# Kernel tuning notes

Measured on AMD Instinct MI355X. Metric: run time of the kernel, lower is better.

## Reference

```python
import jax, jax.numpy as jnp
import numpy as np

HIDDEN = 1024
N_EXPERTS = 8
CAP_FACTOR = 1.1
LN_EPS = 1e-5


def setup_inputs() -> dict:
    key = jax.random.key(0)
    ks = jax.random.split(key, 8)
    d, E, dff = HIDDEN, N_EXPERTS, 4 * HIDDEN
    x = jax.random.normal(ks[0], (4, 2048, d), dtype=jnp.float32)
    gate_w = jax.random.normal(ks[1], (d, E), dtype=jnp.float32) / np.sqrt(d)
    ln_g = jnp.ones((E, d), dtype=jnp.float32)
    ln_b = jnp.zeros((E, d), dtype=jnp.float32)
    w1 = jax.random.normal(ks[2], (E, d, dff), dtype=jnp.float32) / np.sqrt(d)
    b1 = jnp.zeros((E, dff), dtype=jnp.float32)
    w2 = jax.random.normal(ks[3], (E, dff, d), dtype=jnp.float32) / np.sqrt(dff)
    b2 = jnp.zeros((E, d), dtype=jnp.float32)
    return {"x": x, "gate_w": gate_w, "ln_g": ln_g, "ln_b": ln_b,
            "w1": w1, "b1": b1, "w2": w2, "b2": b2}


def reference(x, gate_w, ln_g, ln_b, w1, b1, w2, b2):
    B, S, d = x.shape
    E = gate_w.shape[1]
    N = B * S
    cap = int(N / E * CAP_FACTOR)  # expert capacity

    xt = x.reshape(N, d)
    # Router: top-1 expert per token (max-subtract before softmax is a no-op)
    logits = xt @ gate_w                               # [N, E]
    probs = jax.nn.softmax(logits, axis=-1)
    eidx = jnp.argmax(probs, axis=-1)                  # [N] int

    onehot = jax.nn.one_hot(eidx, E, dtype=jnp.int32)  # [N, E]
    counts = onehot.sum(axis=0).astype(jnp.float32)    # pre-drop counts [E]

    # Deterministic capacity: keep first `cap` tokens per expert, drop rest.
    # (torch code drops randomly via multinomial; structure is identical.)
    pos = jnp.cumsum(onehot, axis=0) - 1               # [N, E]
    pos_tok = jnp.take_along_axis(pos, eidx[:, None], axis=1)[:, 0]  # [N]
    keep = (pos_tok < cap).astype(x.dtype)             # [N]
    pos_c = jnp.minimum(pos_tok, cap - 1)              # clamp; dropped tokens write zeros

    # Dispatch into per-expert buffers [E, cap, d]
    buf = jnp.zeros((E, cap, d), dtype=x.dtype).at[eidx, pos_c].add(xt * keep[:, None])

    # Per-expert FFN: LayerNorm -> Linear -> GELU -> Linear
    mu = buf.mean(axis=-1, keepdims=True)
    var = jnp.mean((buf - mu) ** 2, axis=-1, keepdims=True)
    nb = (buf - mu) * jax.lax.rsqrt(var + LN_EPS)
    nb = nb * ln_g[:, None, :] + ln_b[:, None, :]
    h = jax.nn.gelu(jnp.einsum('ecd,edf->ecf', nb, w1) + b1[:, None, :], approximate=False)
    y = jnp.einsum('ecf,efd->ecd', h, w2) + b2[:, None, :]  # [E, cap, d]

    # Combine: dropped tokens get zeros (matches torch output init)
    out_tok = y[eidx, pos_c] * keep[:, None]           # [N, d]
    output = out_tok.reshape(B, S, d)

    # Load-balancing loss: 1 - cosine(counts, uniform) * 0.01
    tokens_per_expert = N / E
    uniform = jnp.full((E,), tokens_per_expert, dtype=jnp.float32)
    cos = jnp.dot(counts, uniform) / (jnp.linalg.norm(counts) * jnp.linalg.norm(uniform) + 1e-8)
    loss = 1.0 - cos * 0.01
    return output, loss
```

## Files before the change

### kernel.cpp

```cpp
#include <hip/hip_runtime.h>
#include <cstdint>
#include <cstddef>

#define NTOK 8192
#define D    1024
#define DFF  4096
#define NEXP 8
#define CAP  1126
#define MPAD 1152

typedef float f32x4 __attribute__((ext_vector_type(4)));
typedef __bf16 bf16x8 __attribute__((ext_vector_type(8)));

__device__ inline unsigned short f2bf(float f) {
    unsigned u = __float_as_uint(f);
    u += 0x7fffu + ((u >> 16) & 1u);
    return (unsigned short)(u >> 16);
}

__device__ inline void gload16(const void* g, void* l) {
    __builtin_amdgcn_global_load_lds(
        (const __attribute__((address_space(1))) unsigned int*)g,
        (__attribute__((address_space(3))) unsigned int*)l,
        16, 0, 0);
}

__global__ __launch_bounds__(256) void router_kernel(
    const float* __restrict__ x, const float* __restrict__ gw, int* __restrict__ eidx)
{
    int tok  = blockIdx.x * 4 + (threadIdx.x >> 6);
    int lane = threadIdx.x & 63;
    const float* xr = x + (size_t)tok * D;
    float a[8] = {0.f,0.f,0.f,0.f,0.f,0.f,0.f,0.f};
    #pragma unroll
    for (int it = 0; it < D / 64; ++it) {
        int d = lane + it * 64;
        float xv = xr[d];
        const float4 g0 = *(const float4*)(gw + (size_t)d * 8);
        const float4 g1 = *(const float4*)(gw + (size_t)d * 8 + 4);
        a[0] += xv * g0.x; a[1] += xv * g0.y; a[2] += xv * g0.z; a[3] += xv * g0.w;
        a[4] += xv * g1.x; a[5] += xv * g1.y; a[6] += xv * g1.z; a[7] += xv * g1.w;
    }
    #pragma unroll
    for (int off = 32; off > 0; off >>= 1)
        #pragma unroll
        for (int e = 0; e < 8; ++e) a[e] += __shfl_xor(a[e], off, 64);
    if (lane == 0) {
        int bi = 0; float bv = a[0];
        #pragma unroll
        for (int e = 1; e < 8; ++e) if (a[e] > bv) { bv = a[e]; bi = e; }
        eidx[tok] = bi;
    }
}

__global__ __launch_bounds__(1024) void scan_kernel(
    const int* __restrict__ eidx, int* __restrict__ slot_map,
    int* __restrict__ kept_cnt, float* __restrict__ loss_out)
{
    __shared__ int sc[8][1024];
    int t = threadIdx.x;
    int le[8];
    int c[8] = {0,0,0,0,0,0,0,0};
    #pragma unroll
    for (int i = 0; i < 8; ++i) { le[i] = eidx[t * 8 + i]; c[le[i]]++; }
    int v[8];
    #pragma unroll
    for (int e = 0; e < 8; ++e) { v[e] = c[e]; sc[e][t] = v[e]; }
    __syncthreads();
    for (int s = 1; s < 1024; s <<= 1) {
        int add[8] = {0,0,0,0,0,0,0,0};
        if (t >= s) {
            #pragma unroll
            for (int e = 0; e < 8; ++e) add[e] = sc[e][t - s];
        }
        __syncthreads();
        #pragma unroll
        for (int e = 0; e < 8; ++e) { v[e] += add[e]; sc[e][t] = v[e]; }
        __syncthreads();
    }
    int base[8];
    #pragma unroll
    for (int e = 0; e < 8; ++e) base[e] = v[e] - c[e];
    #pragma unroll
    for (int i = 0; i < 8; ++i) {
        int e = le[i]; int pos = base[e]++;
        if (pos < CAP) slot_map[e * CAP + pos] = t * 8 + i;
    }
    if (t == 1023) {
        float dotv = 0.f, ss = 0.f;
        #pragma unroll
        for (int e = 0; e < 8; ++e) {
            float cf = (float)v[e];
            kept_cnt[e] = v[e] < CAP ? v[e] : CAP;
            dotv += cf * 1024.0f;
            ss   += cf * cf;
        }
        float denom = sqrtf(ss) * (1024.0f * sqrtf(8.0f)) + 1e-8f;
        loss_out[0] = 1.0f - 0.01f * (dotv / denom);
    }
}

__global__ __launch_bounds__(256) void zero_out(float4* __restrict__ p, int n)
{
    int stride = gridDim.x * blockDim.x;
    for (int i = blockIdx.x * blockDim.x + threadIdx.x; i < n; i += stride)
        p[i] = make_float4(0.f, 0.f, 0.f, 0.f);
}

__global__ __launch_bounds__(256) void dispatch_ln(
    const float* __restrict__ x, const float* __restrict__ lng, const float* __restrict__ lnb,
    const int* __restrict__ slot_map, const int* __restrict__ kept_cnt,
    unsigned short* __restrict__ xbuf)
{
    int p = blockIdx.x, e = blockIdx.y, tid = threadIdx.x;
    ushort4* dst = (ushort4*)(xbuf + ((size_t)e * MPAD + p) * D) + tid;
    if (p >= kept_cnt[e]) { *dst = make_ushort4(0, 0, 0, 0); return; }
    int tok = slot_map[e * CAP + p];
    const float4 xv = *((const float4*)(x + (size_t)tok * D) + tid);
    float s  = xv.x + xv.y + xv.z + xv.w;
    float ss = xv.x * xv.x + xv.y * xv.y + xv.z * xv.z + xv.w * xv.w;
    #pragma unroll
    for (int off = 32; off > 0; off >>= 1) {
        s  += __shfl_xor(s,  off, 64);
        ss += __shfl_xor(ss, off, 64);
    }
    __shared__ float red[8];
    int lane = tid & 63, wv = tid >> 6;
    if (lane == 0) { red[wv] = s; red[4 + wv] = ss; }
    __syncthreads();
    s  = red[0] + red[1] + red[2] + red[3];
    ss = red[4] + red[5] + red[6] + red[7];
    float mu = s * (1.0f / D);
    float rs = rsqrtf(ss * (1.0f / D) - mu * mu + 1e-5f);
    const float4 gv = *((const float4*)(lng + (size_t)e * D) + tid);
    const float4 bv = *((const float4*)(lnb + (size_t)e * D) + tid);
    ushort4 o;
    o.x = f2bf((xv.x - mu) * rs * gv.x + bv.x);
    o.y = f2bf((xv.y - mu) * rs * gv.y + bv.y);
    o.z = f2bf((xv.z - mu) * rs * gv.z + bv.z);
    o.w = f2bf((xv.w - mu) * rs * gv.w + bv.w);
    *dst = o;
}

__global__ __launch_bounds__(256) void transpose_bf16(
    const float* __restrict__ W, unsigned short* __restrict__ WT, int K, int N)
{
    __shared__ float t[64][65];
    int e = blockIdx.z;
    int n0 = blockIdx.x * 64, k0 = blockIdx.y * 64;
    const float* We = W + (size_t)e * K * N;
    unsigned short* WTe = WT + (size_t)e * K * N;
    int tx = threadIdx.x & 15, ty = threadIdx.x >> 4;
    #pragma unroll
    for (int j = 0; j < 4; ++j) {
        int k = ty + 16 * j;
        const float4 v = *(const float4*)(We + (size_t)(k0 + k) * N + n0 + tx * 4);
        t[k][tx * 4 + 0] = v.x; t[k][tx * 4 + 1] = v.y;
        t[k][tx * 4 + 2] = v.z; t[k][tx * 4 + 3] = v.w;
    }
    __syncthreads();
    #pragma unroll
    for (int j = 0; j < 4; ++j) {
        int n = ty + 16 * j;
        ushort4 o;
        o.x = f2bf(t[tx * 4 + 0][n]); o.y = f2bf(t[tx * 4 + 1][n]);
        o.z = f2bf(t[tx * 4 + 2][n]); o.w = f2bf(t[tx * 4 + 3][n]);
        *(ushort4*)(WTe + (size_t)(n0 + n) * K + k0 + tx * 4) = o;
    }
}

template<int K, int N, int MODE>
__global__ __launch_bounds__(256, 2) void gemm_kernel(
    const unsigned short* __restrict__ A,
    const unsigned short* __restrict__ BT,
    const float* __restrict__ bias,
    unsigned short* __restrict__ Hout,
    float* __restrict__ Yout,
    const int* __restrict__ slot_map,
    const int* __restrict__ kept_cnt)
{
    constexpr int MB = MPAD / 128;
    constexpr int NB = N / 128;
    const int T = NEXP * MB * NB;
    const int orig = blockIdx.x;
    const int q8 = T >> 3, r8 = T & 7;
    const int xcd = orig & 7, ii = orig >> 3;
    const int swz = (xcd < r8 ? xcd * (q8 + 1) : r8 * (q8 + 1) + (xcd - r8) * q8) + ii;
    const int mb = swz % MB;
    const int t2 = swz / MB;
    const int nb = t2 % NB;
    const int e  = t2 / NB;

    const int tid  = threadIdx.x;
    const int lane = tid & 63;
    const int l15  = lane & 15, lg = lane >> 4;
    const int wave = tid >> 6, wr = wave >> 1, wc = wave & 1;
    __shared__ __align__(16) char smem[32768];
    const unsigned short* Ae = A + ((size_t)e * MPAD + (size_t)mb * 128) * K;
    const unsigned short* Be = BT + ((size_t)e * N + (size_t)nb * 128) * K;
    f32x4 acc[4][4] = {};

    auto stage = [&](int buf, int kk) {
        char* sA = smem + buf * 16384;
        char* sB = sA + 8192;
        #pragma unroll
        for (int q = 0; q < 2; ++q) {
            int cid = q * 256 + tid;
            int row = cid >> 2, pp = cid & 3;
            int cc  = pp ^ ((row >> 1) & 3);
            gload16(Ae + (size_t)row * K + kk * 32 + cc * 8, sA + cid * 16);
            gload16(Be + (size_t)row * K + kk * 32 + cc * 8, sB + cid * 16);
        }
    };
    auto compute = [&](int buf) {
        const char* sA = smem + buf * 16384;
        const char* sB = sA + 8192;
        bf16x8 af[4], bfr[4];
        #pragma unroll
        for (int i = 0; i < 4; ++i) {
            int ra = wr * 64 + i * 16 + l15;
            af[i]  = *(const bf16x8*)(sA + ra * 64 + ((lg ^ ((ra >> 1) & 3)) << 4));
            int rb = wc * 64 + i * 16 + l15;
            bfr[i] = *(const bf16x8*)(sB + rb * 64 + ((lg ^ ((rb >> 1) & 3)) << 4));
        }
        #pragma unroll
        for (int mi = 0; mi < 4; ++mi)
            #pragma unroll
            for (int ni = 0; ni < 4; ++ni)
                acc[mi][ni] = __builtin_amdgcn_mfma_f32_16x16x32_bf16(
                    af[mi], bfr[ni], acc[mi][ni], 0, 0, 0);
    };

    stage(0, 0);
    asm volatile("s_waitcnt vmcnt(0)" ::: "memory");
    __syncthreads();
    int cur = 0;
    for (int kk = 0; kk + 1 < K / 32; ++kk) {
        stage(cur ^ 1, kk + 1);
        compute(cur);
        asm volatile("s_waitcnt vmcnt(0)" ::: "memory");
        __syncthreads();
        cur ^= 1;
    }
    compute(cur);

    const int kept = (MODE == 1) ? kept_cnt[e] : 0;
    #pragma unroll
    for (int mi = 0; mi < 4; ++mi) {
        #pragma unroll
        for (int ni = 0; ni < 4; ++ni) {
            int col = nb * 128 + wc * 64 + ni * 16 + l15;
            float bv = bias[(size_t)e * N + col];
            #pragma unroll
            for (int j = 0; j < 4; ++j) {
                int row = mb * 128 + wr * 64 + mi * 16 + 4 * lg + j;
                float v = acc[mi][ni][j] + bv;
                if (MODE == 0) {
                    v = 0.5f * v * (1.0f + erff(v * 0.70710678118654752f));
                    Hout[((size_t)e * MPAD + row) * N + col] = f2bf(v);
                } else {
                    if (row < kept) {
                        int tok = slot_map[e * CAP + row];
                        Yout[(size_t)tok * D + col] = v;
                    }
                }
            }
        }
    }
}

extern "C" void kernel_launch(void* const* d_in, const int* in_sizes, int n_in,
                              void* d_out, int out_size, void* d_ws, size_t ws_size,
                              hipStream_t stream)
{
    const float* x   = (const float*)d_in[0];
    const float* gw  = (const float*)d_in[1];
    const float* lng = (const float*)d_in[2];
    const float* lnb = (const float*)d_in[3];
    const float* w1  = (const float*)d_in[4];
    const float* b1  = (const float*)d_in[5];
    const float* w2  = (const float*)d_in[6];
    const float* b2  = (const float*)d_in[7];
    float* out = (float*)d_out;

    char* ws = (char*)d_ws;
    unsigned short* wT   = (unsigned short*)ws;
    unsigned short* xbuf = (unsigned short*)(ws + 67108864);
    unsigned short* hbuf = (unsigned short*)(ws + 67108864 + 18874368);
    int* eidx     = (int*)(ws + 161480704);
    int* slot_map = eidx + NTOK;
    int* kept     = slot_map + NEXP * CAP;

    router_kernel<<<NTOK / 4, 256, 0, stream>>>(x, gw, eidx);
    scan_kernel<<<1, 1024, 0, stream>>>(eidx, slot_map, kept, out + (size_t)NTOK * D);
    zero_out<<<2048, 256, 0, stream>>>((float4*)out, NTOK * D / 4);
    dispatch_ln<<<dim3(MPAD, NEXP), 256, 0, stream>>>(x, lng, lnb, slot_map, kept, xbuf);

    transpose_bf16<<<dim3(DFF / 64, D / 64, NEXP), 256, 0, stream>>>(w1, wT, D, DFF);
    gemm_kernel<D, DFF, 0><<<NEXP * (MPAD / 128) * (DFF / 128), 256, 0, stream>>>(
        xbuf, wT, b1, hbuf, nullptr, slot_map, kept);

    transpose_bf16<<<dim3(D / 64, DFF / 64, NEXP), 256, 0, stream>>>(w2, wT, DFF, D);
    gemm_kernel<DFF, D, 1><<<NEXP * (MPAD / 128) * (D / 128), 256, 0, stream>>>(
        hbuf, wT, b2, nullptr, out, slot_map, kept);
}
```

Baseline: 336.1 us.

## Fold W2 transpose into GEMM1 grid and triple-buffer GEMM K loop

Two changes touch the GEMM kernel. The W2 fp32-to-bf16 transpose now runs as extra trailing blocks of the first GEMM launch, writing into a separate workspace region, so it can overlap with GEMM1 work and one launch is saved. The K loop moves from double to triple buffering in LDS (48KB shared) with partial vmcnt waits, and the MFMA section is wrapped in s_setprio. The larger LDS footprint may reduce occupancy, and the fused path only runs when the workspace is big enough for the second transposed weight buffer.

```diff
diff --git a/kernel.cpp b/kernel.cpp
--- a/kernel.cpp
+++ b/kernel.cpp
@@ -169,7 +169,7 @@
     }
 }
 
-template<int K, int N, int MODE>
+template<int K, int N, int MODE, bool FUSET>
 __global__ __launch_bounds__(256, 2) void gemm_kernel(
     const unsigned short* __restrict__ A,
     const unsigned short* __restrict__ BT,
@@ -177,13 +177,45 @@
     unsigned short* __restrict__ Hout,
     float* __restrict__ Yout,
     const int* __restrict__ slot_map,
-    const int* __restrict__ kept_cnt)
+    const int* __restrict__ kept_cnt,
+    const float* __restrict__ tW,
+    unsigned short* __restrict__ tWT)
 {
     constexpr int MB = MPAD / 128;
     constexpr int NB = N / 128;
-    const int T = NEXP * MB * NB;
+    constexpr int GB = NEXP * MB * NB;
+    __shared__ __align__(16) char smem[49152];
+
+    if (FUSET && blockIdx.x >= GB) {
+        int tb = blockIdx.x - GB;
+        int bx = tb & 15, by = (tb >> 4) & 63, e = tb >> 10;
+        float (*tt)[65] = (float(*)[65])smem;
+        int n0 = bx * 64, k0 = by * 64;
+        const float* We = tW + (size_t)e * DFF * D;
+        unsigned short* WTe = tWT + (size_t)e * DFF * D;
+        int tx = threadIdx.x & 15, ty = threadIdx.x >> 4;
+        #pragma unroll
+        for (int j = 0; j < 4; ++j) {
+            int k = ty + 16 * j;
+            const float4 v = *(const float4*)(We + (size_t)(k0 + k) * D + n0 + tx * 4);
+            tt[k][tx * 4 + 0] = v.x; tt[k][tx * 4 + 1] = v.y;
+            tt[k][tx * 4 + 2] = v.z; tt[k][tx * 4 + 3] = v.w;
+        }
+        __syncthreads();
+        #pragma unroll
+        for (int j = 0; j < 4; ++j) {
+            int n = ty + 16 * j;
+            ushort4 o;
+            o.x = f2bf(tt[tx * 4 + 0][n]); o.y = f2bf(tt[tx * 4 + 1][n]);
+            o.z = f2bf(tt[tx * 4 + 2][n]); o.w = f2bf(tt[tx * 4 + 3][n]);
+            *(ushort4*)(WTe + (size_t)(n0 + n) * DFF + k0 + tx * 4) = o;
+        }
+        return;
+    }
+
+    const int T8 = GB;
     const int orig = blockIdx.x;
-    const int q8 = T >> 3, r8 = T & 7;
+    const int q8 = T8 >> 3, r8 = T8 & 7;
     const int xcd = orig & 7, ii = orig >> 3;
     const int swz = (xcd < r8 ? xcd * (q8 + 1) : r8 * (q8 + 1) + (xcd - r8) * q8) + ii;
     const int mb = swz % MB;
@@ -195,7 +227,6 @@
     const int lane = tid & 63;
     const int l15  = lane & 15, lg = lane >> 4;
     const int wave = tid >> 6, wr = wave >> 1, wc = wave & 1;
-    __shared__ __align__(16) char smem[32768];
     const unsigned short* Ae = A + ((size_t)e * MPAD + (size_t)mb * 128) * K;
     const unsigned short* Be = BT + ((size_t)e * N + (size_t)nb * 128) * K;
     f32x4 acc[4][4] = {};
@@ -223,26 +254,38 @@
             int rb = wc * 64 + i * 16 + l15;
             bfr[i] = *(const bf16x8*)(sB + rb * 64 + ((lg ^ ((rb >> 1) & 3)) << 4));
         }
+        __builtin_amdgcn_s_setprio(1);
         #pragma unroll
         for (int mi = 0; mi < 4; ++mi)
             #pragma unroll
             for (int ni = 0; ni < 4; ++ni)
                 acc[mi][ni] = __builtin_amdgcn_mfma_f32_16x16x32_bf16(
                     af[mi], bfr[ni], acc[mi][ni], 0, 0, 0);
+        __builtin_amdgcn_s_setprio(0);
     };
 
+    constexpr int T = K / 32;
     stage(0, 0);
-    asm volatile("s_waitcnt vmcnt(0)" ::: "memory");
-    __syncthreads();
-    int cur = 0;
-    for (int kk = 0; kk + 1 < K / 32; ++kk) {
-        stage(cur ^ 1, kk + 1);
-        compute(cur);
-        asm volatile("s_waitcnt vmcnt(0)" ::: "memory");
-        __syncthreads();
-        cur ^= 1;
-    }
-    compute(cur);
+    stage(1, 1);
+    asm volatile("s_waitcnt vmcnt(4)" ::: "memory");
+    __builtin_amdgcn_s_barrier();
+    asm volatile("" ::: "memory");
+    int b = 0;
+    for (int t = 0; t < T - 2; ++t) {
+        int bn = b + 2; if (bn >= 3) bn -= 3;
+        stage(bn, t + 2);
+        compute(b);
+        asm volatile("s_waitcnt vmcnt(4) lgkmcnt(0)" ::: "memory");
+        __builtin_amdgcn_s_barrier();
+        asm volatile("" ::: "memory");
+        b = (b == 2) ? 0 : b + 1;
+    }
+    compute(b);
+    asm volatile("s_waitcnt vmcnt(0) lgkmcnt(0)" ::: "memory");
+    __builtin_amdgcn_s_barrier();
+    asm volatile("" ::: "memory");
+    b = (b == 2) ? 0 : b + 1;
+    compute(b);
 
     const int kept = (MODE == 1) ? kept_cnt[e] : 0;
     #pragma unroll
@@ -284,23 +327,35 @@
     float* out = (float*)d_out;
 
     char* ws = (char*)d_ws;
-    unsigned short* wT   = (unsigned short*)ws;
+    unsigned short* wT1  = (unsigned short*)ws;
     unsigned short* xbuf = (unsigned short*)(ws + 67108864);
     unsigned short* hbuf = (unsigned short*)(ws + 67108864 + 18874368);
     int* eidx     = (int*)(ws + 161480704);
     int* slot_map = eidx + NTOK;
     int* kept     = slot_map + NEXP * CAP;
+    const size_t OFF_WT2 = 161549568;
+    unsigned short* wT2 = (unsigned short*)(ws + OFF_WT2);
+    const bool fuse = (ws_size >= OFF_WT2 + 67108864ULL);
+
+    constexpr int GB1 = NEXP * (MPAD / 128) * (DFF / 128);
+    constexpr int GB2 = NEXP * (MPAD / 128) * (D / 128);
 
     router_kernel<<<NTOK / 4, 256, 0, stream>>>(x, gw, eidx);
     scan_kernel<<<1, 1024, 0, stream>>>(eidx, slot_map, kept, out + (size_t)NTOK * D);
     zero_out<<<2048, 256, 0, stream>>>((float4*)out, NTOK * D / 4);
     dispatch_ln<<<dim3(MPAD, NEXP), 256, 0, stream>>>(x, lng, lnb, slot_map, kept, xbuf);
 
-    transpose_bf16<<<dim3(DFF / 64, D / 64, NEXP), 256, 0, stream>>>(w1, wT, D, DFF);
-    gemm_kernel<D, DFF, 0><<<NEXP * (MPAD / 128) * (DFF / 128), 256, 0, stream>>>(
-        xbuf, wT, b1, hbuf, nullptr, slot_map, kept);
-
-    transpose_bf16<<<dim3(D / 64, DFF / 64, NEXP), 256, 0, stream>>>(w2, wT, DFF, D);
-    gemm_kernel<DFF, D, 1><<<NEXP * (MPAD / 128) * (D / 128), 256, 0, stream>>>(
-        hbuf, wT, b2, nullptr, out, slot_map, kept);
-}
+    transpose_bf16<<<dim3(DFF / 64, D / 64, NEXP), 256, 0, stream>>>(w1, wT1, D, DFF);
+    if (fuse) {
+        gemm_kernel<D, DFF, 0, true><<<GB1 + 8192, 256, 0, stream>>>(
+            xbuf, wT1, b1, hbuf, nullptr, slot_map, kept, w2, wT2);
+        gemm_kernel<DFF, D, 1, false><<<GB2, 256, 0, stream>>>(
+            hbuf, wT2, b2, nullptr, out, slot_map, kept, nullptr, nullptr);
+    } else {
+        gemm_kernel<D, DFF, 0, false><<<GB1, 256, 0, stream>>>(
+            xbuf, wT1, b1, hbuf, nullptr, slot_map, kept, nullptr, nullptr);
+        transpose_bf16<<<dim3(D / 64, DFF / 64, NEXP), 256, 0, stream>>>(w2, wT1, DFF, D);
+        gemm_kernel<DFF, D, 1, false><<<GB2, 256, 0, stream>>>(
+            hbuf, wT1, b2, nullptr, out, slot_map, kept, nullptr, nullptr);
+    }
+}
```

Measured after the change: 339.8 us. Within noise of the previous version (+1.1%).

## Fold w2 transpose into first GEMM launch, vectorize epilogues, zero only dropped rows

Applied to the files above, without the earlier changes.

When the workspace is large enough, the w2 bf16 transpose tiles run as extra blocks of the first GEMM grid, so they overlap with GEMM1 work and a kernel launch is removed. Full-output zeroing is replaced by zeroing only the rows of dropped tokens, which the scan kernel now records in a drop list. The MFMA operands are swapped so each lane holds four consecutive columns. This lets the epilogues use float4 bias loads, ushort4/float4 stores and one slot_map lookup per row. It also swaps erff for a polynomial erf approximation and rewrites the transpose with 128x128 tiles, at the cost of slight GELU accuracy loss and a dependence on workspace size.

```diff
diff --git a/kernel.cpp b/kernel.cpp
--- a/kernel.cpp
+++ b/kernel.cpp
@@ -18,11 +18,67 @@
     return (unsigned short)(u >> 16);
 }
 
+__device__ inline float gelu(float x) {
+    float z  = 0.70710678118654752f * x;
+    float az = fabsf(z);
+    float t  = 1.0f / fmaf(0.3275911f, az, 1.0f);
+    float p  = t * fmaf(t, fmaf(t, fmaf(t, fmaf(t, 1.061405429f, -1.453152027f),
+                                        1.421413741f), -0.284496736f), 0.254829592f);
+    float ee = __expf(-az * az);
+    float er = fmaf(-p, ee, 1.0f);
+    er = __builtin_copysignf(er, z);
+    return 0.5f * x * (1.0f + er);
+}
+
 __device__ inline void gload16(const void* g, void* l) {
     __builtin_amdgcn_global_load_lds(
         (const __attribute__((address_space(1))) unsigned int*)g,
         (__attribute__((address_space(3))) unsigned int*)l,
         16, 0, 0);
+}
+
+__device__ void transpose_tile_dev(const float* __restrict__ W, unsigned short* __restrict__ WT,
+                                   int K, int N, int tb, char* smem)
+{
+    int tiles_k = K >> 7, tiles_n = N >> 7;
+    int per_e = tiles_k * tiles_n;
+    int e = tb / per_e, rem = tb % per_e;
+    int kb = rem % tiles_k, nb = rem / tiles_k;
+    const float* We = W + (size_t)e * K * N + (size_t)(kb * 128) * N + nb * 128;
+    unsigned short* Oe = WT + (size_t)e * K * N + (size_t)(nb * 128) * K + kb * 128;
+    float* lds = (float*)smem;
+    int t = threadIdx.x;
+    #pragma unroll
+    for (int p = 0; p < 2; ++p) {
+        __syncthreads();
+        #pragma unroll
+        for (int j = 0; j < 8; ++j) {
+            int idx = j * 256 + t;
+            int r = idx >> 5, c4 = idx & 31;
+            const float4 v = *(const float4*)(We + (size_t)(p * 64 + r) * N + c4 * 4);
+            *(float4*)(lds + r * 128 + c4 * 4) = v;
+        }
+        __syncthreads();
+        int c = t >> 1, half = t & 1;
+        const float* col = lds + (half * 32) * 128 + c;
+        unsigned short* orow = Oe + (size_t)c * K + p * 64 + half * 32;
+        #pragma unroll
+        for (int q = 0; q < 4; ++q) {
+            uint4 o;
+            o.x = f2bf(col[(q*8+0)*128]) | ((unsigned)f2bf(col[(q*8+1)*128]) << 16);
+            o.y = f2bf(col[(q*8+2)*128]) | ((unsigned)f2bf(col[(q*8+3)*128]) << 16);
+            o.z = f2bf(col[(q*8+4)*128]) | ((unsigned)f2bf(col[(q*8+5)*128]) << 16);
+            o.w = f2bf(col[(q*8+6)*128]) | ((unsigned)f2bf(col[(q*8+7)*128]) << 16);
+            *(uint4*)(orow + q * 8) = o;
+        }
+    }
+}
+
+__global__ __launch_bounds__(256) void transpose_kernel(
+    const float* __restrict__ W, unsigned short* __restrict__ WT, int K, int N)
+{
+    __shared__ __align__(16) char smem[32768];
+    transpose_tile_dev(W, WT, K, N, blockIdx.x, smem);
 }
 
 __global__ __launch_bounds__(256) void router_kernel(
@@ -55,10 +111,13 @@
 
 __global__ __launch_bounds__(1024) void scan_kernel(
     const int* __restrict__ eidx, int* __restrict__ slot_map,
-    int* __restrict__ kept_cnt, float* __restrict__ loss_out)
+    int* __restrict__ kept_cnt, float* __restrict__ loss_out,
+    int* __restrict__ droplist, int* __restrict__ dropcnt)
 {
     __shared__ int sc[8][1024];
+    __shared__ int dcnt;
     int t = threadIdx.x;
+    if (t == 0) dcnt = 0;
     int le[8];
     int c[8] = {0,0,0,0,0,0,0,0};
     #pragma unroll
@@ -85,7 +144,10 @@
     for (int i = 0; i < 8; ++i) {
         int e = le[i]; int pos = base[e]++;
         if (pos < CAP) slot_map[e * CAP + pos] = t * 8 + i;
-    }
+        else { int s = atomicAdd(&dcnt, 1); droplist[s] = t * 8 + i; }
+    }
+    __syncthreads();
+    if (t == 0) *dropcnt = dcnt;
     if (t == 1023) {
         float dotv = 0.f, ss = 0.f;
         #pragma unroll
@@ -98,6 +160,15 @@
         float denom = sqrtf(ss) * (1024.0f * sqrtf(8.0f)) + 1e-8f;
         loss_out[0] = 1.0f - 0.01f * (dotv / denom);
     }
+}
+
+__global__ __launch_bounds__(256) void zero_dropped(
+    const int* __restrict__ droplist, const int* __restrict__ dropcnt,
+    float4* __restrict__ out)
+{
+    int n = (*dropcnt) * 256;
+    for (int idx = blockIdx.x * 256 + threadIdx.x; idx < n; idx += gridDim.x * 256)
+        out[(size_t)droplist[idx >> 8] * 256 + (idx & 255)] = make_float4(0.f,0.f,0.f,0.f);
 }
 
 __global__ __launch_bounds__(256) void zero_out(float4* __restrict__ p, int n)
@@ -142,33 +213,6 @@
     *dst = o;
 }
 
-__global__ __launch_bounds__(256) void transpose_bf16(
-    const float* __restrict__ W, unsigned short* __restrict__ WT, int K, int N)
-{
-    __shared__ float t[64][65];
-    int e = blockIdx.z;
-    int n0 = blockIdx.x * 64, k0 = blockIdx.y * 64;
-    const float* We = W + (size_t)e * K * N;
-    unsigned short* WTe = WT + (size_t)e * K * N;
-    int tx = threadIdx.x & 15, ty = threadIdx.x >> 4;
-    #pragma unroll
-    for (int j = 0; j < 4; ++j) {
-        int k = ty + 16 * j;
-        const float4 v = *(const float4*)(We + (size_t)(k0 + k) * N + n0 + tx * 4);
-        t[k][tx * 4 + 0] = v.x; t[k][tx * 4 + 1] = v.y;
-        t[k][tx * 4 + 2] = v.z; t[k][tx * 4 + 3] = v.w;
-    }
-    __syncthreads();
-    #pragma unroll
-    for (int j = 0; j < 4; ++j) {
-        int n = ty + 16 * j;
-        ushort4 o;
-        o.x = f2bf(t[tx * 4 + 0][n]); o.y = f2bf(t[tx * 4 + 1][n]);
-        o.z = f2bf(t[tx * 4 + 2][n]); o.w = f2bf(t[tx * 4 + 3][n]);
-        *(ushort4*)(WTe + (size_t)(n0 + n) * K + k0 + tx * 4) = o;
-    }
-}
-
 template<int K, int N, int MODE>
 __global__ __launch_bounds__(256, 2) void gemm_kernel(
     const unsigned short* __restrict__ A,
@@ -177,14 +221,24 @@
     unsigned short* __restrict__ Hout,
     float* __restrict__ Yout,
     const int* __restrict__ slot_map,
-    const int* __restrict__ kept_cnt)
-{
+    const int* __restrict__ kept_cnt,
+    const float* __restrict__ tW,
+    unsigned short* __restrict__ tWT,
+    int tK, int tN, int tcount)
+{
+    __shared__ __align__(16) char smem[32768];
+
+    if (blockIdx.x < tcount) {
+        transpose_tile_dev(tW, tWT, tK, tN, blockIdx.x, smem);
+        return;
+    }
+    const int obid = blockIdx.x - tcount;
+
     constexpr int MB = MPAD / 128;
     constexpr int NB = N / 128;
-    const int T = NEXP * MB * NB;
-    const int orig = blockIdx.x;
-    const int q8 = T >> 3, r8 = T & 7;
-    const int xcd = orig & 7, ii = orig >> 3;
+    constexpr int GB = NEXP * MB * NB;
+    const int q8 = GB >> 3, r8 = GB & 7;
+    const int xcd = obid & 7, ii = obid >> 3;
     const int swz = (xcd < r8 ? xcd * (q8 + 1) : r8 * (q8 + 1) + (xcd - r8) * q8) + ii;
     const int mb = swz % MB;
     const int t2 = swz / MB;
@@ -195,7 +249,6 @@
     const int lane = tid & 63;
     const int l15  = lane & 15, lg = lane >> 4;
     const int wave = tid >> 6, wr = wave >> 1, wc = wave & 1;
-    __shared__ __align__(16) char smem[32768];
     const unsigned short* Ae = A + ((size_t)e * MPAD + (size_t)mb * 128) * K;
     const unsigned short* Be = BT + ((size_t)e * N + (size_t)nb * 128) * K;
     f32x4 acc[4][4] = {};
@@ -228,7 +281,7 @@
             #pragma unroll
             for (int ni = 0; ni < 4; ++ni)
                 acc[mi][ni] = __builtin_amdgcn_mfma_f32_16x16x32_bf16(
-                    af[mi], bfr[ni], acc[mi][ni], 0, 0, 0);
+                    bfr[ni], af[mi], acc[mi][ni], 0, 0, 0);
     };
 
     stage(0, 0);
@@ -247,23 +300,27 @@
     const int kept = (MODE == 1) ? kept_cnt[e] : 0;
     #pragma unroll
     for (int mi = 0; mi < 4; ++mi) {
+        const int row = mb * 128 + wr * 64 + mi * 16 + l15;
+        int tok = 0; bool live = true;
+        if (MODE == 1) {
+            live = row < kept;
+            tok = live ? slot_map[e * CAP + row] : 0;
+        }
         #pragma unroll
         for (int ni = 0; ni < 4; ++ni) {
-            int col = nb * 128 + wc * 64 + ni * 16 + l15;
-            float bv = bias[(size_t)e * N + col];
-            #pragma unroll
-            for (int j = 0; j < 4; ++j) {
-                int row = mb * 128 + wr * 64 + mi * 16 + 4 * lg + j;
-                float v = acc[mi][ni][j] + bv;
-                if (MODE == 0) {
-                    v = 0.5f * v * (1.0f + erff(v * 0.70710678118654752f));
-                    Hout[((size_t)e * MPAD + row) * N + col] = f2bf(v);
-                } else {
-                    if (row < kept) {
-                        int tok = slot_map[e * CAP + row];
-                        Yout[(size_t)tok * D + col] = v;
-                    }
-                }
+            const int colb = nb * 128 + wc * 64 + ni * 16 + 4 * lg;
+            const float4 bv = *(const float4*)(bias + (size_t)e * N + colb);
+            if (MODE == 0) {
+                ushort4 o;
+                o.x = f2bf(gelu(acc[mi][ni][0] + bv.x));
+                o.y = f2bf(gelu(acc[mi][ni][1] + bv.y));
+                o.z = f2bf(gelu(acc[mi][ni][2] + bv.z));
+                o.w = f2bf(gelu(acc[mi][ni][3] + bv.w));
+                *(ushort4*)(Hout + ((size_t)e * MPAD + row) * N + colb) = o;
+            } else if (live) {
+                float4 o = make_float4(acc[mi][ni][0] + bv.x, acc[mi][ni][1] + bv.y,
+                                       acc[mi][ni][2] + bv.z, acc[mi][ni][3] + bv.w);
+                *(float4*)(Yout + (size_t)tok * D + colb) = o;
             }
         }
     }
@@ -282,25 +339,57 @@
     const float* w2  = (const float*)d_in[6];
     const float* b2  = (const float*)d_in[7];
     float* out = (float*)d_out;
-
     char* ws = (char*)d_ws;
-    unsigned short* wT   = (unsigned short*)ws;
-    unsigned short* xbuf = (unsigned short*)(ws + 67108864);
-    unsigned short* hbuf = (unsigned short*)(ws + 67108864 + 18874368);
-    int* eidx     = (int*)(ws + 161480704);
-    int* slot_map = eidx + NTOK;
-    int* kept     = slot_map + NEXP * CAP;
-
-    router_kernel<<<NTOK / 4, 256, 0, stream>>>(x, gw, eidx);
-    scan_kernel<<<1, 1024, 0, stream>>>(eidx, slot_map, kept, out + (size_t)NTOK * D);
-    zero_out<<<2048, 256, 0, stream>>>((float4*)out, NTOK * D / 4);
-    dispatch_ln<<<dim3(MPAD, NEXP), 256, 0, stream>>>(x, lng, lnb, slot_map, kept, xbuf);
-
-    transpose_bf16<<<dim3(DFF / 64, D / 64, NEXP), 256, 0, stream>>>(w1, wT, D, DFF);
-    gemm_kernel<D, DFF, 0><<<NEXP * (MPAD / 128) * (DFF / 128), 256, 0, stream>>>(
-        xbuf, wT, b1, hbuf, nullptr, slot_map, kept);
-
-    transpose_bf16<<<dim3(D / 64, DFF / 64, NEXP), 256, 0, stream>>>(w2, wT, DFF, D);
-    gemm_kernel<DFF, D, 1><<<NEXP * (MPAD / 128) * (D / 128), 256, 0, stream>>>(
-        hbuf, wT, b2, nullptr, out, slot_map, kept);
-}
+
+    constexpr int GB1 = NEXP * (MPAD / 128) * (DFF / 128);
+    constexpr int GB2 = NEXP * (MPAD / 128) * (D / 128);
+    constexpr int TB  = 2048;
+
+    const bool fuse = (ws_size >= 228626432ULL);
+
+    if (fuse) {
+        unsigned short* wT1  = (unsigned short*)ws;
+        unsigned short* wT2  = (unsigned short*)(ws + 67108864);
+        int* eidx     = (int*)wT2;
+        int* droplist = (int*)wT2 + NTOK;
+        unsigned short* xbuf = (unsigned short*)(ws + 134217728);
+        unsigned short* hbuf = (unsigned short*)(ws + 153092096);
+        int* slot_map = (int*)(ws + 228589568);
+        int* kept     = slot_map + NEXP * CAP;
+        int* dropcnt  = kept + NEXP;
+
+        router_kernel<<<NTOK / 4, 256, 0, stream>>>(x, gw, eidx);
+        scan_kernel<<<1, 1024, 0, stream>>>(eidx, slot_map, kept,
+                                            out + (size_t)NTOK * D, droplist, dropcnt);
+        zero_dropped<<<64, 256, 0, stream>>>(droplist, dropcnt, (float4*)out);
+        dispatch_ln<<<dim3(MPAD, NEXP), 256, 0, stream>>>(x, lng, lnb, slot_map, kept, xbuf);
+
+        transpose_kernel<<<TB, 256, 0, stream>>>(w1, wT1, D, DFF);
+        gemm_kernel<D, DFF, 0><<<TB + GB1, 256, 0, stream>>>(
+            xbuf, wT1, b1, hbuf, nullptr, slot_map, kept, w2, wT2, DFF, D, TB);
+        gemm_kernel<DFF, D, 1><<<GB2, 256, 0, stream>>>(
+            hbuf, wT2, b2, nullptr, out, slot_map, kept, nullptr, nullptr, 0, 0, 0);
+    } else {
+        unsigned short* wT   = (unsigned short*)ws;
+        unsigned short* xbuf = (unsigned short*)(ws + 67108864);
+        unsigned short* hbuf = (unsigned short*)(ws + 67108864 + 18874368);
+        int* eidx     = (int*)(ws + 161480704);
+        int* slot_map = eidx + NTOK;
+        int* kept     = slot_map + NEXP * CAP;
+        int* dropcnt  = kept + NEXP;
+        int* droplist = (int*)hbuf;
+
+        router_kernel<<<NTOK / 4, 256, 0, stream>>>(x, gw, eidx);
+        scan_kernel<<<1, 1024, 0, stream>>>(eidx, slot_map, kept,
+                                            out + (size_t)NTOK * D, droplist, dropcnt);
+        zero_out<<<2048, 256, 0, stream>>>((float4*)out, NTOK * D / 4);
+        dispatch_ln<<<dim3(MPAD, NEXP), 256, 0, stream>>>(x, lng, lnb, slot_map, kept, xbuf);
+
+        transpose_kernel<<<TB, 256, 0, stream>>>(w1, wT, D, DFF);
+        gemm_kernel<D, DFF, 0><<<GB1, 256, 0, stream>>>(
+            xbuf, wT, b1, hbuf, nullptr, slot_map, kept, nullptr, nullptr, 0, 0, 0);
+        transpose_kernel<<<TB, 256, 0, stream>>>(w2, wT, DFF, D);
+        gemm_kernel<DFF, D, 1><<<GB2, 256, 0, stream>>>(
+            hbuf, wT, b2, nullptr, out, slot_map, kept, nullptr, nullptr, 0, 0, 0);
+    }
+}
```

New measurement: 344.2 us. 1.02x slower.
